# Kernel optimization log

Hardware: AMD Instinct MI355X
Metric: run time of the kernel (lower is better)

The kernel has to match this reference:

```python
import jax, jax.numpy as jnp
import numpy as np

SEQ = 400      # hardcoded per-batch node count in head_splitter
HEADS = 10     # hardcoded num_heads
EPS = 1e-5     # torch LayerNorm default eps


def setup_inputs() -> dict:
    key = jax.random.key(0)
    ks = jax.random.split(key, 6)
    in_dim = out_dim = 640
    N = 25600  # 64 batches * 400 nodes
    x = jax.random.normal(ks[0], (N, in_dim), dtype=jnp.float32)
    # nn.Linear(in, out, bias=False) weights have shape [out, in]; y = x @ W.T
    s = 1.0 / np.sqrt(in_dim)
    Wq = jax.random.uniform(ks[1], (out_dim, in_dim), jnp.float32, -s, s)
    Wk = jax.random.uniform(ks[2], (out_dim, in_dim), jnp.float32, -s, s)
    Wv = jax.random.uniform(ks[3], (out_dim, in_dim), jnp.float32, -s, s)
    gamma = jnp.ones((out_dim,), jnp.float32)
    beta = jnp.zeros((out_dim,), jnp.float32)
    return {"x": x, "Wq": Wq, "Wk": Wk, "Wv": Wv, "gamma": gamma, "beta": beta}


def reference(x, Wq, Wk, Wv, gamma, beta):
    N, D = x.shape
    B = N // SEQ
    dk = D // HEADS
    Q = x @ Wq.T
    K = x @ Wk.T
    V = x @ Wv.T
    # head_splitter: per-batch raw reshape [SEQ, D] -> (HEADS, SEQ, dk), stacked
    # == raw reshape of the full contiguous tensor [N, D] -> (B, HEADS, SEQ, dk)
    Qh = Q.reshape(B, HEADS, SEQ, dk)
    Vh = V.reshape(B, HEADS, SEQ, dk)
    # NOTE: original uses torch.reshape (NOT transpose) to get (B, H, dk, SEQ)
    Kh = K.reshape(B, HEADS, SEQ, dk).reshape(B, HEADS, dk, SEQ)
    scale = 1.0 / jnp.sqrt(jnp.float32(dk))
    scores = jnp.einsum('bhqd,bhdk->bhqk', Qh, Kh) * scale  # [B,H,SEQ,SEQ]
    w = jax.nn.softmax(scores, axis=-1)
    vals = jnp.einsum('bhqk,bhkd->bhqd', w, Vh)  # [B,H,SEQ,dk]
    # raw row-major reshape back to [N, D], as in the original
    y = vals.reshape(N, D) + x
    mu = jnp.mean(y, axis=-1, keepdims=True)
    var = jnp.mean(jnp.square(y - mu), axis=-1, keepdims=True)
    return (y - mu) * jax.lax.rsqrt(var + EPS) * gamma + beta
```

## Files before the change

kernel.cpp:

```cpp
#include <hip/hip_runtime.h>
#include <hip/hip_bf16.h>


typedef unsigned short u16;
typedef short s8v __attribute__((ext_vector_type(8)));
typedef float f4v __attribute__((ext_vector_type(4)));
typedef u16  u4v __attribute__((ext_vector_type(4)));
typedef u16  u8v __attribute__((ext_vector_type(8)));

__device__ __forceinline__ float us2f(u16 u) {
    union { float f; unsigned int i; } v; v.i = ((unsigned int)u) << 16; return v.f;
}
__device__ __forceinline__ u16 f2us(float f) {
    __hip_bfloat16 h = __float2bfloat16(f);
    return *reinterpret_cast<u16*>(&h);
}
__device__ __forceinline__ s8v ld8f(const float* p) {
    const float4 a = ((const float4*)p)[0], b = ((const float4*)p)[1];
    s8v r;
    r[0] = (short)f2us(a.x); r[1] = (short)f2us(a.y);
    r[2] = (short)f2us(a.z); r[3] = (short)f2us(a.w);
    r[4] = (short)f2us(b.x); r[5] = (short)f2us(b.y);
    r[6] = (short)f2us(b.z); r[7] = (short)f2us(b.w);
    return r;
}
__device__ __forceinline__ void gload16(const u16* g, u16* l) {
    u16* gm = const_cast<u16*>(g);
    __builtin_amdgcn_global_load_lds(
        (__attribute__((address_space(1))) unsigned int*)gm,
        (__attribute__((address_space(3))) unsigned int*)l, 16, 0, 0);
}


__global__ __launch_bounds__(256)
void cvt(const float* __restrict__ Wq, const float* __restrict__ Wk,
         const float* __restrict__ Wv, const float* __restrict__ x,
         u16* __restrict__ Wb, u16* __restrict__ xb)
{
    const int g = blockIdx.x * 256 + threadIdx.x;
    if (g < 153600) {
        const float* src = (g < 51200) ? Wq : (g < 102400) ? Wk : Wv;
        const int rem = g % 51200;
        *(s8v*)(Wb + (size_t)g * 8) = ld8f(src + (size_t)rem * 8);
    } else {
        const int gx = g - 153600;
        *(s8v*)(xb + (size_t)gx * 8) = ld8f(x + (size_t)gx * 8);
    }
}

__global__ __launch_bounds__(256, 4)
void qkv(const u16* __restrict__ xb, const u16* __restrict__ Wb,
         u16* __restrict__ Qb, u16* __restrict__ Kb, u16* __restrict__ Vb)
{
    __shared__ u16 As[8192], Bs[8192];
    const int bx = blockIdx.x;
    const int mt = bx % 200, nt = bx / 200;
    const int m0 = mt * 128, n0 = nt * 128;
    const int t = threadIdx.x, lane = t & 63, w = t >> 6;
    const int l15 = lane & 15, quad = lane >> 4;
    const int wr = w >> 1, wc = w & 1;

    f4v acc[4][4];
    #pragma unroll
    for (int a = 0; a < 4; ++a)
        #pragma unroll
        for (int b = 0; b < 4; ++b) acc[a][b] = (f4v){0.f, 0.f, 0.f, 0.f};

    for (int k0 = 0; k0 < 640; k0 += 64) {
        __syncthreads();
        #pragma unroll
        for (int j = 0; j < 4; ++j) {
            const int c  = (w * 4 + j) * 64 + lane;
            const int rg = c >> 3;
            const int sg = (c & 7) ^ (rg & 7);
            gload16(xb + (size_t)(m0 + rg) * 640 + k0 + sg * 8,
                    As + (w * 4 + j) * 512);
            gload16(Wb + (size_t)(n0 + rg) * 640 + k0 + sg * 8,
                    Bs + (w * 4 + j) * 512);
        }
        __syncthreads();

        #pragma unroll
        for (int kk = 0; kk < 2; ++kk) {
            s8v af[4], bf[4];
            #pragma unroll
            for (int mi = 0; mi < 4; ++mi) {
                const int row = wr * 64 + mi * 16 + l15;
                const int s   = kk * 4 + quad;
                af[mi] = *(const s8v*)(As + ((row * 8 + (s ^ (row & 7))) << 3));
            }
            #pragma unroll
            for (int ni = 0; ni < 4; ++ni) {
                const int row = wc * 64 + ni * 16 + l15;
                const int s   = kk * 4 + quad;
                bf[ni] = *(const s8v*)(Bs + ((row * 8 + (s ^ (row & 7))) << 3));
            }
            #pragma unroll
            for (int mi = 0; mi < 4; ++mi)
                #pragma unroll
                for (int ni = 0; ni < 4; ++ni)
                    acc[mi][ni] = __builtin_amdgcn_mfma_f32_16x16x32_bf16(
                        af[mi], bf[ni], acc[mi][ni], 0, 0, 0);
        }
    }

    const int mat = (n0 >= 1280) ? 2 : (n0 >= 640 ? 1 : 0);
    u16* dst = (mat == 0) ? Qb : (mat == 1 ? Kb : Vb);
    const int lc = n0 - mat * 640 + wc * 64;
    #pragma unroll
    for (int mi = 0; mi < 4; ++mi)
        #pragma unroll
        for (int ni = 0; ni < 4; ++ni)
            #pragma unroll
            for (int i = 0; i < 4; ++i) {
                const int row = m0 + wr * 64 + mi * 16 + quad * 4 + i;
                dst[(size_t)row * 640 + lc + ni * 16 + l15] = f2us(acc[mi][ni][i]);
            }
}

__global__ __launch_bounds__(256)
void kvt(const u16* __restrict__ Kb, const u16* __restrict__ Vb,
         u16* __restrict__ Ktg, u16* __restrict__ Vtg)
{
    extern __shared__ u16 sm[];
    const int bh = blockIdx.x, t = threadIdx.x;
    {
        const u16* src = Kb + (size_t)bh * 25600;
        for (int c = t; c < 3200; c += 256) {
            const int d = c / 50, k8 = (c % 50) * 8;
            *(s8v*)(sm + ((d * 512 + k8) ^ (((d >> 3) & 7) << 3))) =
                *(const s8v*)(src + (size_t)c * 8);
        }
        __syncthreads();
        u16* o = Ktg + (size_t)bh * 25600;
        for (int c = t; c < 3200; c += 256) {
            const int key = c >> 3, d0 = (c & 7) * 8;
            u8v v;
            #pragma unroll
            for (int j = 0; j < 8; ++j) {
                const int d = d0 + j;
                v[j] = sm[(d * 512 + key) ^ (((d >> 3) & 7) << 3)];
            }
            *(u8v*)(o + key * 64 + d0) = v;
        }
    }
    __syncthreads();
    {
        const u16* src = Vb + (size_t)bh * 25600;
        for (int c = t; c < 3200; c += 256) {
            const int key = c >> 3, d0 = (c & 7) * 8;
            *(s8v*)(sm + ((key * 64 + d0) ^ (((key >> 3) & 7) << 3))) =
                *(const s8v*)(src + (size_t)c * 8);
        }
        __syncthreads();
        u16* o = Vtg + (size_t)bh * 26624;
        for (int c = t; c < 3584; c += 256) {
            const int d = ((c >> 3) & 7) + (((c >> 6) & 7) << 3);
            const int s = (c & 7) + ((c >> 9) << 3);
            if (s >= 52) continue;
            const int key0 = s * 8;
            u8v v;
            #pragma unroll
            for (int j = 0; j < 8; ++j) {
                const int key = key0 + j;
                v[j] = (key < 400)
                     ? sm[(key * 64 + d) ^ (((key >> 3) & 7) << 3)] : (u16)0;
            }
            *(u8v*)(o + d * 416 + key0) = v;
        }
    }
}

#define ATTN_LDS 44320
__global__ __launch_bounds__(512, 6)
void attn(const u16* __restrict__ Qb, const u16* __restrict__ Ktg,
          const u16* __restrict__ Vtg, const float* __restrict__ x,
          const float* __restrict__ gamma, const float* __restrict__ beta,
          float* __restrict__ out)
{
    extern __shared__ char smem[];
    u16*   Pb  = (u16*)smem;
    float* Vl  = (float*)(smem + 33920);
    float* rs_ = (float*)(smem + 44160);

    const int bx = blockIdx.x;
    const int sw = (bx & 7) * 800 + (bx >> 3);
    const int bh = sw / 10, qc = sw % 10;
    const int t = threadIdx.x, lane = t & 63, w = t >> 6;
    const int l15 = lane & 15, quad = lane >> 4;
    const size_t kbase = (size_t)bh * 25600;
    const size_t vbase = (size_t)bh * 26624;
    const size_t qoff0 = kbase + (size_t)qc * 2560;
    const int M0[3] = {0, 16, 24};

    s8v qf[3][2];
    #pragma unroll
    for (int mt = 0; mt < 3; ++mt)
        #pragma unroll
        for (int kq = 0; kq < 2; ++kq)
            qf[mt][kq] = *(const s8v*)(Qb + qoff0
                         + (size_t)(M0[mt] + l15) * 64 + kq * 32 + quad * 8);

    int nts[4]; int nn = 0;
    for (int nt = w; nt < 25; nt += 8) nts[nn++] = nt;
    s8v k0c, k1c;
    {
        const u16* kp = Ktg + kbase + (size_t)(nts[0] * 16 + l15) * 64 + quad * 8;
        k0c = *(const s8v*)(kp); k1c = *(const s8v*)(kp + 32);
    }
    #pragma unroll
    for (int j = 0; j < 4; ++j) {
        if (j >= nn) break;
        s8v k0n = k0c, k1n = k1c;
        if (j + 1 < nn) {
            const u16* kp = Ktg + kbase
                          + (size_t)(nts[j + 1] * 16 + l15) * 64 + quad * 8;
            k0n = *(const s8v*)(kp); k1n = *(const s8v*)(kp + 32);
        }
        const int nt = nts[j];
        #pragma unroll
        for (int mt = 0; mt < 3; ++mt) {
            f4v acc = (f4v){0.f, 0.f, 0.f, 0.f};
            acc = __builtin_amdgcn_mfma_f32_16x16x32_bf16(qf[mt][0], k0c, acc, 0, 0, 0);
            acc = __builtin_amdgcn_mfma_f32_16x16x32_bf16(qf[mt][1], k1c, acc, 0, 0, 0);
            #pragma unroll
            for (int i = 0; i < 4; ++i)
                Pb[(M0[mt] + quad * 4 + i) * 424 + nt * 16 + l15] =
                    f2us(acc[i] * 0.125f);
        }
        k0c = k0n; k1c = k1n;
    }
    __syncthreads();

    for (int q = w; q < 40; q += 8) {
        const int c0 = lane * 8;
        float sv[8]; float m = -1e30f;
        if (c0 < 424) {
            const s8v pv = *(const s8v*)(Pb + q * 424 + c0);
            #pragma unroll
            for (int j = 0; j < 8; ++j) {
                sv[j] = (c0 + j < 400) ? us2f((u16)pv[j]) : -1e30f;
                m = fmaxf(m, sv[j]);
            }
        } else {
            #pragma unroll
            for (int j = 0; j < 8; ++j) sv[j] = -1e30f;
        }
        #pragma unroll
        for (int off = 32; off; off >>= 1) m = fmaxf(m, __shfl_xor(m, off));
        float s = 0.f;
        if (c0 < 424) {
            u8v ev;
            #pragma unroll
            for (int j = 0; j < 8; ++j) {
                const float e = (c0 + j < 400) ? __expf(sv[j] - m) : 0.f;
                s += e; ev[j] = f2us(e);
            }
            *(u8v*)(Pb + q * 424 + c0) = ev;
        }
        #pragma unroll
        for (int off = 32; off; off >>= 1) s += __shfl_xor(s, off);
        if (lane == 0) rs_[q] = s;
    }
    __syncthreads();

    {
        const int ntv = w & 3;
        const int mA  = w >> 2;
        const bool two = (mA == 0);
        f4v acc0 = (f4v){0.f, 0.f, 0.f, 0.f};
        f4v acc1 = (f4v){0.f, 0.f, 0.f, 0.f};
        const u16* vp  = Vtg + vbase + (size_t)(ntv * 16 + l15) * 416 + quad * 8;
        const u16* pa  = Pb + (M0[mA] + l15) * 424 + quad * 8;
        const u16* pa2 = Pb + (24 + l15) * 424 + quad * 8;
        s8v bc  = *(const s8v*)(vp);
        s8v p0c = *(const s8v*)(pa);
        s8v p2c = two ? *(const s8v*)(pa2) : p0c;
        #pragma unroll
        for (int k0 = 0; k0 < 416; k0 += 32) {
            s8v bn = bc, p0n = p0c, p2n = p2c;
            if (k0 + 32 < 416) {
                bn  = *(const s8v*)(vp + k0 + 32);
                p0n = *(const s8v*)(pa + k0 + 32);
                if (two) p2n = *(const s8v*)(pa2 + k0 + 32);
            }
            acc0 = __builtin_amdgcn_mfma_f32_16x16x32_bf16(p0c, bc, acc0, 0, 0, 0);
            if (two)
                acc1 = __builtin_amdgcn_mfma_f32_16x16x32_bf16(p2c, bc, acc1, 0, 0, 0);
            bc = bn; p0c = p0n; p2c = p2n;
        }
        #pragma unroll
        for (int i = 0; i < 4; ++i) {
            Vl[(M0[mA] + quad * 4 + i) * 64 + ntv * 16 + l15] = acc0[i];
            if (two) Vl[(24 + quad * 4 + i) * 64 + ntv * 16 + l15] = acc1[i];
        }
    }
    __syncthreads();

    if (w < 4) {
        const size_t grow = ((size_t)bh * 40 + qc * 4 + w) * 640;
        float xv[10], vl[10], rr[10], gv[10], bv[10];
        #pragma unroll
        for (int ci = 0; ci < 10; ++ci) {
            const int col = lane + 64 * ci;
            xv[ci] = x[grow + col];
            gv[ci] = gamma[col];
            bv[ci] = beta[col];
            vl[ci] = Vl[w * 640 + col];
            rr[ci] = rs_[w * 10 + ci];
        }
        float y[10], s = 0.f, ss = 0.f;
        #pragma unroll
        for (int ci = 0; ci < 10; ++ci) {
            const float v = vl[ci] / rr[ci] + xv[ci];
            y[ci] = v; s += v; ss += v * v;
        }
        #pragma unroll
        for (int off = 32; off; off >>= 1) {
            s += __shfl_xor(s, off); ss += __shfl_xor(ss, off);
        }
        const float mu = s * (1.f / 640.f);
        float var = ss * (1.f / 640.f) - mu * mu;
        var = fmaxf(var, 0.f);
        const float rstd = rsqrtf(var + 1e-5f);
        #pragma unroll
        for (int ci = 0; ci < 10; ++ci) {
            const int col = lane + 64 * ci;
            out[grow + col] = (y[ci] - mu) * rstd * gv[ci] + bv[ci];
        }
    }
}

#define LDS_BYTES 163712

template<int MODE>
__global__ __launch_bounds__(1024, 4)
void mha(const float* __restrict__ x,
         const float* __restrict__ Wq, const float* __restrict__ Wk,
         const float* __restrict__ Wv,
         const float* __restrict__ gamma, const float* __restrict__ beta,
         float* __restrict__ out,
         const u16* __restrict__ Wb, u16* __restrict__ Qb)
{
    extern __shared__ char smem[];
    u16*   Kt  = (u16*)(smem);
    u16*   Vt  = (u16*)(smem + 57600);
    u16*   Xs  = (u16*)(smem + 111872);
    u16*   Pb  = (u16*)(smem + 111872);
    float* Vl  = (float*)(smem + 145792);
    float* rs_ = (float*)(smem + 156032);

    const int    bh   = blockIdx.x;
    const size_t base = (size_t)bh * 25600;
    const int    t    = threadIdx.x;
    const int    lane = t & 63;
    const int    w    = t >> 6;
    const int    l15  = lane & 15;
    const int    quad = lane >> 4;

    for (int i = t; i < 6400; i += 1024) {
        const int row = i / 160, col = (i % 160) * 4;
        const float4 v = *(const float4*)(x + base + row * 640 + col);
        *(u4v*)(Xs + row * 648 + col) =
            (u4v){f2us(v.x), f2us(v.y), f2us(v.z), f2us(v.w)};
    }
    for (int i = t; i < 64 * 24; i += 1024)
        Vt[(i / 24) * 424 + 400 + (i % 24)] = 0;
    __syncthreads();

    {
        const int M0a[3] = {0, 16, 24};
        int nts[3], nnt = 0;
        for (int nt = w; nt < 40; nt += 16) nts[nnt++] = nt;

        for (int zi = 0; zi < 3; ++zi) {
            const float* Wsrc = (zi == 0) ? Wq : (zi == 1) ? Wk : Wv;
            f4v acc[3][3];
            #pragma unroll
            for (int a = 0; a < 3; ++a)
                #pragma unroll
                for (int b = 0; b < 3; ++b) acc[a][b] = (f4v){0.f,0.f,0.f,0.f};

            for (int k0 = 0; k0 < 640; k0 += 32) {
                s8v afr[3];
                #pragma unroll
                for (int mt = 0; mt < 3; ++mt)
                    afr[mt] = *(const s8v*)(Xs + (M0a[mt] + l15) * 648 + k0 + quad * 8);
                #pragma unroll
                for (int nk = 0; nk < 3; ++nk) {
                    if (nk >= nnt) break;
                    const int nt = nts[nk];
                    s8v bfr;
                    if (MODE == 0)
                        bfr = *(const s8v*)(Wb + (size_t)zi * 409600
                                            + (nt * 16 + l15) * 640 + k0 + quad * 8);
                    else
                        bfr = ld8f(Wsrc + (size_t)(nt * 16 + l15) * 640 + k0 + quad * 8);
                    #pragma unroll
                    for (int mt = 0; mt < 3; ++mt)
                        acc[nk][mt] = __builtin_amdgcn_mfma_f32_16x16x32_bf16(
                            afr[mt], bfr, acc[nk][mt], 0, 0, 0);
                }
            }
            #pragma unroll
            for (int nk = 0; nk < 3; ++nk) {
                if (nk >= nnt) break;
                #pragma unroll
                for (int mt = 0; mt < 3; ++mt)
                    #pragma unroll
                    for (int i = 0; i < 4; ++i) {
                        const int r  = M0a[mt] + quad * 4 + i;
                        const int oc = nts[nk] * 16 + l15;
                        const int f  = r * 640 + oc;
                        const float v = acc[nk][mt][i];
                        if (zi == 0) {
                            if (MODE == 0) Qb[base + f] = f2us(v);
                            else           out[base + f] = v;
                        } else if (zi == 1) {
                            const int d = f / 400, key = f - d * 400;
                            Kt[key * 72 + d] = f2us(v);
                        } else {
                            Vt[(f & 63) * 424 + (f >> 6)] = f2us(v);
                        }
                    }
            }
        }
    }
    __syncthreads();

    const int M0b[3] = {0, 16, 24};
    for (int qc = 0; qc < 10; ++qc) {
        for (int nt = w; nt < 25; nt += 16) {
            s8v bfr[2];
            #pragma unroll
            for (int kq = 0; kq < 2; ++kq)
                bfr[kq] = *(const s8v*)(Kt + (nt * 16 + l15) * 72 + kq * 32 + quad * 8);
            #pragma unroll
            for (int mt = 0; mt < 3; ++mt) {
                f4v acc = (f4v){0.f, 0.f, 0.f, 0.f};
                #pragma unroll
                for (int kq = 0; kq < 2; ++kq) {
                    const size_t qoff = base + (size_t)qc * 2560
                                      + (M0b[mt] + l15) * 64 + kq * 32 + quad * 8;
                    s8v a = (MODE == 0) ? *(const s8v*)(Qb + qoff) : ld8f(out + qoff);
                    acc = __builtin_amdgcn_mfma_f32_16x16x32_bf16(a, bfr[kq], acc, 0, 0, 0);
                }
                #pragma unroll
                for (int i = 0; i < 4; ++i)
                    Pb[(M0b[mt] + quad * 4 + i) * 424 + nt * 16 + l15] =
                        f2us(acc[i] * 0.125f);
            }
        }
        __syncthreads();

        for (int q = w; q < 40; q += 16) {
            float sv[7], m = -1e30f;
            #pragma unroll
            for (int ii = 0; ii < 7; ++ii) {
                const int c = lane + ii * 64;
                sv[ii] = (c < 400) ? us2f(Pb[q * 424 + c]) : -1e30f;
                m = fmaxf(m, sv[ii]);
            }
            #pragma unroll
            for (int off = 32; off; off >>= 1) m = fmaxf(m, __shfl_xor(m, off));
            float s = 0.f;
            #pragma unroll
            for (int ii = 0; ii < 7; ++ii) {
                const int c = lane + ii * 64;
                const float e = (c < 400) ? __expf(sv[ii] - m) : 0.f;
                s += e;
                if (c < 424) Pb[q * 424 + c] = f2us(e);
            }
            #pragma unroll
            for (int off = 32; off; off >>= 1) s += __shfl_xor(s, off);
            if (lane == 0) rs_[q] = s;
        }
        __syncthreads();

        if (w < 12) {
            const int mt = w >> 2, nt = w & 3;
            f4v acc = (f4v){0.f, 0.f, 0.f, 0.f};
            for (int k0 = 0; k0 < 416; k0 += 32) {
                s8v a = *(const s8v*)(Pb + (M0b[mt] + l15) * 424 + k0 + quad * 8);
                s8v b = *(const s8v*)(Vt + (nt * 16 + l15) * 424 + k0 + quad * 8);
                acc = __builtin_amdgcn_mfma_f32_16x16x32_bf16(a, b, acc, 0, 0, 0);
            }
            #pragma unroll
            for (int i = 0; i < 4; ++i)
                Vl[(M0b[mt] + quad * 4 + i) * 64 + nt * 16 + l15] = acc[i];
        }
        __syncthreads();

        if (w < 4) {
            const int    r    = qc * 4 + w;
            const size_t grow = base + (size_t)r * 640;
            float y[10], s = 0.f, ss = 0.f;
            #pragma unroll
            for (int ci = 0; ci < 10; ++ci) {
                const int col = lane + 64 * ci;
                const float v = Vl[w * 640 + col] / rs_[w * 10 + ci] + x[grow + col];
                y[ci] = v; s += v; ss += v * v;
            }
            #pragma unroll
            for (int off = 32; off; off >>= 1) {
                s += __shfl_xor(s, off); ss += __shfl_xor(ss, off);
            }
            const float mu = s * (1.f / 640.f);
            float var = ss * (1.f / 640.f) - mu * mu;
            var = fmaxf(var, 0.f);
            const float rstd = rsqrtf(var + 1e-5f);
            #pragma unroll
            for (int ci = 0; ci < 10; ++ci) {
                const int col = lane + 64 * ci;
                out[grow + col] = (y[ci] - mu) * rstd * gamma[col] + beta[col];
            }
        }
    }
}

__global__ __launch_bounds__(256)
void wconv(const float* __restrict__ Wq, const float* __restrict__ Wk,
           const float* __restrict__ Wv, u16* __restrict__ Wb)
{
    const int g = blockIdx.x * 256 + threadIdx.x;
    const float* src = (g < 51200) ? Wq : (g < 102400) ? Wk : Wv;
    const int rem = g % 51200;
    *(s8v*)(Wb + (size_t)g * 8) = ld8f(src + (size_t)rem * 8);
}

extern "C" void kernel_launch(void* const* d_in, const int* in_sizes, int n_in,
                              void* d_out, int out_size, void* d_ws, size_t ws_size,
                              hipStream_t stream)
{
    const float* x     = (const float*)d_in[0];
    const float* Wq    = (const float*)d_in[1];
    const float* Wk    = (const float*)d_in[2];
    const float* Wv    = (const float*)d_in[3];
    const float* gamma = (const float*)d_in[4];
    const float* beta  = (const float*)d_in[5];
    float* out = (float*)d_out;
    (void)in_sizes; (void)n_in; (void)out_size;

    hipFuncSetAttribute(reinterpret_cast<const void*>(&kvt),
                        hipFuncAttributeMaxDynamicSharedMemorySize, 65536);
    hipFuncSetAttribute(reinterpret_cast<const void*>(&attn),
                        hipFuncAttributeMaxDynamicSharedMemorySize, ATTN_LDS);
    hipFuncSetAttribute(reinterpret_cast<const void*>(&mha<0>),
                        hipFuncAttributeMaxDynamicSharedMemorySize, LDS_BYTES);
    hipFuncSetAttribute(reinterpret_cast<const void*>(&mha<1>),
                        hipFuncAttributeMaxDynamicSharedMemorySize, LDS_BYTES);

    const size_t NEED_NEW = 200376320ull;

    if (ws_size >= NEED_NEW) {
        u16* Wb  = (u16*)d_ws;
        u16* xb  = Wb  + 1228800;
        u16* Qb  = xb  + 16384000;
        u16* Kb  = Qb  + 16384000;
        u16* Vb  = Kb  + 16384000;
        u16* Ktg = Vb  + 16384000;
        u16* Vtg = Ktg + 16384000;
        cvt <<<8600, 256, 0, stream>>>(Wq, Wk, Wv, x, Wb, xb);
        qkv <<<3000, 256, 0, stream>>>(xb, Wb, Qb, Kb, Vb);
        kvt <<<640,  256, 65536, stream>>>(Kb, Vb, Ktg, Vtg);
        attn<<<6400, 512, ATTN_LDS, stream>>>(Qb, Ktg, Vtg, x, gamma, beta, out);
    } else if (ws_size >= (size_t)(2457600 + 32768000)) {
        u16* Wb = (u16*)d_ws;
        u16* Qb = Wb + 1228800;
        wconv<<<600, 256, 0, stream>>>(Wq, Wk, Wv, Wb);
        mha<0><<<640, 1024, LDS_BYTES, stream>>>(x, Wq, Wk, Wv, gamma, beta, out, Wb, Qb);
    } else {
        mha<1><<<640, 1024, LDS_BYTES, stream>>>(x, Wq, Wk, Wv, gamma, beta, out,
                                                 (const u16*)d_ws, (u16*)d_ws);
    }
}
```

Before: 357.5 us.

## Stage QKV epilogue through LDS, swizzle tiles, batch softmax rows, deepen PV prefetch

The QKV GEMM now writes its bf16 output tile to shared memory first and then stores it to global memory as 16-byte coalesced rows, replacing the scattered 2-byte stores. Block indices are remapped so blocks running together cover tiles in an XCD-friendly order. In the attention kernel, the residual x is loaded early to hide its latency, softmax processes five rows per wave at once so the shuffle reductions interleave, and the PV loop uses a three-deep register prefetch. These changes raise register use and LDS allocation in exchange for better coalescing and latency hiding.

```diff
diff --git a/kernel.cpp b/kernel.cpp
--- a/kernel.cpp
+++ b/kernel.cpp
@@ -48,13 +48,17 @@
     }
 }
 
+#define QKV_LDS 36864
 __global__ __launch_bounds__(256, 4)
 void qkv(const u16* __restrict__ xb, const u16* __restrict__ Wb,
          u16* __restrict__ Qb, u16* __restrict__ Kb, u16* __restrict__ Vb)
 {
-    __shared__ u16 As[8192], Bs[8192];
+    extern __shared__ u16 qsm[];
+    u16* As = qsm;
+    u16* Bs = qsm + 8192;
     const int bx = blockIdx.x;
-    const int mt = bx % 200, nt = bx / 200;
+    const int sw = (bx & 7) * 375 + (bx >> 3);
+    const int mt = sw / 15, nt = sw % 15;
     const int m0 = mt * 128, n0 = nt * 128;
     const int t = threadIdx.x, lane = t & 63, w = t >> 6;
     const int l15 = lane & 15, quad = lane >> 4;
@@ -104,18 +108,29 @@
         }
     }
 
+    __syncthreads();
+    u16* Cs = qsm;
+    #pragma unroll
+    for (int mi = 0; mi < 4; ++mi)
+        #pragma unroll
+        for (int ni = 0; ni < 4; ++ni)
+            #pragma unroll
+            for (int i = 0; i < 4; ++i) {
+                const int row = wr * 64 + mi * 16 + quad * 4 + i;
+                const int col = wc * 64 + ni * 16 + l15;
+                Cs[row * 144 + col] = f2us(acc[mi][ni][i]);
+            }
+    __syncthreads();
     const int mat = (n0 >= 1280) ? 2 : (n0 >= 640 ? 1 : 0);
     u16* dst = (mat == 0) ? Qb : (mat == 1 ? Kb : Vb);
-    const int lc = n0 - mat * 640 + wc * 64;
+    const int lc0 = n0 - mat * 640;
     #pragma unroll
-    for (int mi = 0; mi < 4; ++mi)
-        #pragma unroll
-        for (int ni = 0; ni < 4; ++ni)
-            #pragma unroll
-            for (int i = 0; i < 4; ++i) {
-                const int row = m0 + wr * 64 + mi * 16 + quad * 4 + i;
-                dst[(size_t)row * 640 + lc + ni * 16 + l15] = f2us(acc[mi][ni][i]);
-            }
+    for (int j2 = 0; j2 < 8; ++j2) {
+        const int cl  = t + 256 * j2;
+        const int row = cl >> 4, cg = cl & 15;
+        const s8v v = *(const s8v*)(Cs + row * 144 + cg * 8);
+        *(s8v*)(dst + (size_t)(m0 + row) * 640 + lc0 + cg * 8) = v;
+    }
 }
 
 __global__ __launch_bounds__(256)
@@ -193,6 +208,13 @@
     const size_t qoff0 = kbase + (size_t)qc * 2560;
     const int M0[3] = {0, 16, 24};
 
+    const size_t grow = ((size_t)bh * 40 + qc * 4 + w) * 640;
+    float xpre[10];
+    if (w < 4) {
+        #pragma unroll
+        for (int ci = 0; ci < 10; ++ci) xpre[ci] = x[grow + lane + 64 * ci];
+    }
+
     s8v qf[3][2];
     #pragma unroll
     for (int mt = 0; mt < 3; ++mt)
@@ -232,35 +254,54 @@
     }
     __syncthreads();
 
-    for (int q = w; q < 40; q += 8) {
-        const int c0 = lane * 8;
-        float sv[8]; float m = -1e30f;
-        if (c0 < 424) {
-            const s8v pv = *(const s8v*)(Pb + q * 424 + c0);
-            #pragma unroll
-            for (int j = 0; j < 8; ++j) {
-                sv[j] = (c0 + j < 400) ? us2f((u16)pv[j]) : -1e30f;
-                m = fmaxf(m, sv[j]);
-            }
-        } else {
-            #pragma unroll
-            for (int j = 0; j < 8; ++j) sv[j] = -1e30f;
-        }
-        #pragma unroll
-        for (int off = 32; off; off >>= 1) m = fmaxf(m, __shfl_xor(m, off));
-        float s = 0.f;
-        if (c0 < 424) {
-            u8v ev;
-            #pragma unroll
-            for (int j = 0; j < 8; ++j) {
-                const float e = (c0 + j < 400) ? __expf(sv[j] - m) : 0.f;
-                s += e; ev[j] = f2us(e);
-            }
-            *(u8v*)(Pb + q * 424 + c0) = ev;
-        }
-        #pragma unroll
-        for (int off = 32; off; off >>= 1) s += __shfl_xor(s, off);
-        if (lane == 0) rs_[q] = s;
+    {
+        const int  c0  = lane * 8;
+        const bool act = (c0 < 424);
+        s8v pv[5];
+        #pragma unroll
+        for (int r = 0; r < 5; ++r)
+            if (act) pv[r] = *(const s8v*)(Pb + (w + r * 8) * 424 + c0);
+        float mx[5];
+        #pragma unroll
+        for (int r = 0; r < 5; ++r) {
+            float m = -1e30f;
+            if (act) {
+                #pragma unroll
+                for (int j = 0; j < 8; ++j)
+                    if (c0 + j < 400) m = fmaxf(m, us2f((u16)pv[r][j]));
+            }
+            mx[r] = m;
+        }
+        #pragma unroll
+        for (int off = 32; off; off >>= 1)
+            #pragma unroll
+            for (int r = 0; r < 5; ++r)
+                mx[r] = fmaxf(mx[r], __shfl_xor(mx[r], off));
+        float sm5[5];
+        #pragma unroll
+        for (int r = 0; r < 5; ++r) {
+            float s = 0.f;
+            if (act) {
+                u8v ev;
+                #pragma unroll
+                for (int j = 0; j < 8; ++j) {
+                    const float e = (c0 + j < 400)
+                                  ? __expf(us2f((u16)pv[r][j]) - mx[r]) : 0.f;
+                    s += e; ev[j] = f2us(e);
+                }
+                *(u8v*)(Pb + (w + r * 8) * 424 + c0) = ev;
+            }
+            sm5[r] = s;
+        }
+        #pragma unroll
+        for (int off = 32; off; off >>= 1)
+            #pragma unroll
+            for (int r = 0; r < 5; ++r)
+                sm5[r] += __shfl_xor(sm5[r], off);
+        if (lane == 0) {
+            #pragma unroll
+            for (int r = 0; r < 5; ++r) rs_[w + r * 8] = sm5[r];
+        }
     }
     __syncthreads();
 
@@ -273,21 +314,25 @@
         const u16* vp  = Vtg + vbase + (size_t)(ntv * 16 + l15) * 416 + quad * 8;
         const u16* pa  = Pb + (M0[mA] + l15) * 424 + quad * 8;
         const u16* pa2 = Pb + (24 + l15) * 424 + quad * 8;
-        s8v bc  = *(const s8v*)(vp);
-        s8v p0c = *(const s8v*)(pa);
-        s8v p2c = two ? *(const s8v*)(pa2) : p0c;
-        #pragma unroll
-        for (int k0 = 0; k0 < 416; k0 += 32) {
-            s8v bn = bc, p0n = p0c, p2n = p2c;
-            if (k0 + 32 < 416) {
-                bn  = *(const s8v*)(vp + k0 + 32);
-                p0n = *(const s8v*)(pa + k0 + 32);
-                if (two) p2n = *(const s8v*)(pa2 + k0 + 32);
-            }
-            acc0 = __builtin_amdgcn_mfma_f32_16x16x32_bf16(p0c, bc, acc0, 0, 0, 0);
+        s8v vb[3], pb0[3], pb2[3];
+        #pragma unroll
+        for (int kp = 0; kp < 3; ++kp) {
+            vb[kp]  = *(const s8v*)(vp  + kp * 32);
+            pb0[kp] = *(const s8v*)(pa  + kp * 32);
+            pb2[kp] = *(const s8v*)(pa2 + kp * 32);
+        }
+        #pragma unroll
+        for (int k = 0; k < 13; ++k) {
+            const int s = k % 3;
+            const s8v b = vb[s], p0 = pb0[s], p2 = pb2[s];
+            if (k + 3 < 13) {
+                vb[s]  = *(const s8v*)(vp  + (k + 3) * 32);
+                pb0[s] = *(const s8v*)(pa  + (k + 3) * 32);
+                pb2[s] = *(const s8v*)(pa2 + (k + 3) * 32);
+            }
+            acc0 = __builtin_amdgcn_mfma_f32_16x16x32_bf16(p0, b, acc0, 0, 0, 0);
             if (two)
-                acc1 = __builtin_amdgcn_mfma_f32_16x16x32_bf16(p2c, bc, acc1, 0, 0, 0);
-            bc = bn; p0c = p0n; p2c = p2n;
+                acc1 = __builtin_amdgcn_mfma_f32_16x16x32_bf16(p2, b, acc1, 0, 0, 0);
         }
         #pragma unroll
         for (int i = 0; i < 4; ++i) {
@@ -298,12 +343,10 @@
     __syncthreads();
 
     if (w < 4) {
-        const size_t grow = ((size_t)bh * 40 + qc * 4 + w) * 640;
-        float xv[10], vl[10], rr[10], gv[10], bv[10];
+        float vl[10], rr[10], gv[10], bv[10];
         #pragma unroll
         for (int ci = 0; ci < 10; ++ci) {
             const int col = lane + 64 * ci;
-            xv[ci] = x[grow + col];
             gv[ci] = gamma[col];
             bv[ci] = beta[col];
             vl[ci] = Vl[w * 640 + col];
@@ -312,7 +355,7 @@
         float y[10], s = 0.f, ss = 0.f;
         #pragma unroll
         for (int ci = 0; ci < 10; ++ci) {
-            const float v = vl[ci] / rr[ci] + xv[ci];
+            const float v = vl[ci] / rr[ci] + xpre[ci];
             y[ci] = v; s += v; ss += v * v;
         }
         #pragma unroll
@@ -541,6 +584,8 @@
     float* out = (float*)d_out;
     (void)in_sizes; (void)n_in; (void)out_size;
 
+    hipFuncSetAttribute(reinterpret_cast<const void*>(&qkv),
+                        hipFuncAttributeMaxDynamicSharedMemorySize, QKV_LDS);
     hipFuncSetAttribute(reinterpret_cast<const void*>(&kvt),
                         hipFuncAttributeMaxDynamicSharedMemorySize, 65536);
     hipFuncSetAttribute(reinterpret_cast<const void*>(&attn),
@@ -561,7 +606,7 @@
         u16* Ktg = Vb  + 16384000;
         u16* Vtg = Ktg + 16384000;
         cvt <<<8600, 256, 0, stream>>>(Wq, Wk, Wv, x, Wb, xb);
-        qkv <<<3000, 256, 0, stream>>>(xb, Wb, Qb, Kb, Vb);
+        qkv <<<3000, 256, QKV_LDS, stream>>>(xb, Wb, Qb, Kb, Vb);
         kvt <<<640,  256, 65536, stream>>>(Kb, Vb, Ktg, Vtg);
         attn<<<6400, 512, ATTN_LDS, stream>>>(Qb, Ktg, Vtg, x, gamma, beta, out);
     } else if (ws_size >= (size_t)(2457600 + 32768000)) {
```

New measurement: 403.4 us. +12.8%, slower.
